# Kernel optimization log

Hardware: AMD Instinct MI355X
Metric: run time of the kernel (lower is better)

## Reference

```python
import math
import jax, jax.numpy as jnp
from jax import lax
import numpy as np

C, H, W, N, K = 256, 64, 64, 16, 7

def setup_inputs() -> dict:
    key = jax.random.key(0)
    k0, k1, k2, k3, k4 = jax.random.split(key, 5)
    x = jax.random.normal(k0, (N, C, H, W), dtype=jnp.float32)
    p_2_w = 0.02 * jax.random.normal(k1, (1, C, H, 1), dtype=jnp.float32)
    # nn.Conv2d(c, c, (1,5), groups=1, bias=False) -> weight [c, c, 1, 5]
    fan_in = C * 1 * 5
    bound = 1.0 / math.sqrt(fan_in)
    p_3_w = jax.random.uniform(k2, (C, C, 1, 5), dtype=jnp.float32, minval=-bound, maxval=bound)
    p_4_w = 0.02 * jax.random.normal(k3, (1, C, K, 1, 1), dtype=jnp.float32)
    p_6_w = jax.random.uniform(k4, (K, 1), dtype=jnp.float32, minval=-7.0, maxval=7.0)
    return {"x": x, "p_2_w": p_2_w, "p_3_w": p_3_w, "p_4_w": p_4_w, "p_6_w": p_6_w}

def reference(x, p_2_w, p_3_w, p_4_w, p_6_w):
    n, c, h, w = x.shape
    k = p_4_w.shape[2]  # 7 taps
    pad = (k - 1) // 2
    # F.unfold with kernel (1,7), pad (0,3): stack 7 width-shifted copies -> [n,c,7,h,w]
    xp = jnp.pad(x, ((0, 0), (0, 0), (0, 0), (pad, pad)))
    t_1 = jnp.stack([xp[..., i:i + w] for i in range(k)], axis=2)
    # per-(channel,row) scaling then dense 1x5 conv
    t_2 = p_2_w * x
    t_3 = lax.conv_general_dilated(
        t_2, p_3_w, window_strides=(1, 1), padding=[(0, 0), (2, 2)],
        dimension_numbers=("NCHW", "OIHW", "NCHW"))
    # weighted tap-sum: (p_4_w * t_1) contracted over taps with p_6_w[:,0]
    t_4 = p_4_w * t_1
    t_6 = jnp.einsum("nckhw,kf->ncfhw", t_4, p_6_w)[:, :, 0]  # [n,c,h,w]
    t_5 = jax.nn.relu(x)
    s = h * w
    # channel-attention matrix [n,c,c]
    t_7 = jnp.einsum("ncs,nds->ncd", t_3.reshape(n, c, s), t_6.reshape(n, c, s))
    t_7 = t_7 * (1.0 / math.sqrt(s))
    # bmm(t_5^T, t_7) -> [n,s,d]; permuting to [n,d,h,w] == einsum 'ncs,ncd->nds'
    out = jnp.einsum("ncs,ncd->nds", t_5.reshape(n, c, s), t_7)
    out = out * (1.0 / math.sqrt(c))
    return out.reshape(n, c, h, w)
```

## Files before the change

### kernel.cpp

```cpp
#include <hip/hip_runtime.h>
#include <hip/hip_bf16.h>

typedef __attribute__((ext_vector_type(8))) short bf16x8;
typedef __attribute__((ext_vector_type(4))) float f32x4;

#define NB 16
#define CD 256
#define HD 64
#define WD 64
#define WP 68
#define SD 4096
#define KU 1280

__device__ __forceinline__ void gload16(const void* g, void* lds) {
  __builtin_amdgcn_global_load_lds(
      (const __attribute__((address_space(1))) unsigned int*)g,
      (__attribute__((address_space(3))) unsigned int*)lds, 16, 0, 0);
}

__global__ __launch_bounds__(256) void prep_w3(const float* __restrict__ p3,
                                               __hip_bfloat16* __restrict__ A) {
  int id = blockIdx.x * 256 + threadIdx.x;
  if (id >= CD * KU) return;
  int o = id / KU;
  int r = id - o * KU;
  int j = r >> 8;
  int c = r & 255;
  A[id] = __float2bfloat16(p3[(o * CD + c) * 5 + j]);
}

__global__ __launch_bounds__(256) void prep_x(const float* __restrict__ x,
                                              const float* __restrict__ p2,
                                              const float* __restrict__ p4,
                                              const float* __restrict__ p6,
                                              __hip_bfloat16* __restrict__ t2p,
                                              __hip_bfloat16* __restrict__ t5T,
                                              __hip_bfloat16* __restrict__ t6) {
  int h = blockIdx.x;
  int c0 = blockIdx.y * 64;
  int n = blockIdx.z;
  __shared__ float xl[64][67];
  __shared__ float p2l[64];
  __shared__ float wtl[64][8];
  int t = threadIdx.x;

  if (t < 64) p2l[t] = p2[(c0 + t) * HD + h];
  for (int idx = t; idx < 448; idx += 256) {
    int c = idx / 7, k = idx - c * 7;
    wtl[c][k] = p4[(c0 + c) * 7 + k] * p6[k];
  }

  {
    int cq = t >> 4;
    int w4 = (t & 15) * 4;
#pragma unroll
    for (int cc = 0; cc < 4; ++cc) {
      int cl = cc * 16 + cq;
      const float4 xv = *reinterpret_cast<const float4*>(
          &x[(((size_t)n * CD + c0 + cl) * HD + h) * WD + w4]);
      xl[cl][w4 + 0] = xv.x;
      xl[cl][w4 + 1] = xv.y;
      xl[cl][w4 + 2] = xv.z;
      xl[cl][w4 + 3] = xv.w;
    }
  }
  __syncthreads();

  __hip_bfloat16* t2pn = t2p + (size_t)n * HD * WP * CD;
#pragma unroll
  for (int ii = 0; ii < 2; ++ii) {
    int w = (t >> 3) + ii * 32;
    int cb = (t & 7) * 8;
    __hip_bfloat16 o2[8], o5[8];
#pragma unroll
    for (int j = 0; j < 8; ++j) {
      float xv = xl[cb + j][w];
      o5[j] = __float2bfloat16(fmaxf(xv, 0.f));
      o2[j] = __float2bfloat16(p2l[cb + j] * xv);
    }
    size_t s = (size_t)h * 64 + w;
    *reinterpret_cast<bf16x8*>(&t5T[((size_t)n * SD + s) * CD + c0 + cb]) =
        *reinterpret_cast<const bf16x8*>(o5);
    *reinterpret_cast<bf16x8*>(&t2pn[((size_t)h * WP + w + 2) * CD + c0 + cb]) =
        *reinterpret_cast<const bf16x8*>(o2);
  }
  if (t < 32) {
    int pi = t >> 3;
    int wp = (pi < 2) ? pi : pi + 64;
    int cb = (t & 7) * 8;
    bf16x8 z = (bf16x8){0, 0, 0, 0, 0, 0, 0, 0};
    *reinterpret_cast<bf16x8*>(&t2pn[((size_t)h * WP + wp) * CD + c0 + cb]) = z;
  }

#pragma unroll
  for (int ii = 0; ii < 2; ++ii) {
    int cl = (t >> 3) + ii * 32;
    int w8 = (t & 7) * 8;
    float hx[14];
#pragma unroll
    for (int m = 0; m < 14; ++m) {
      int wi = w8 - 3 + m;
      hx[m] = (wi >= 0 && wi < 64) ? xl[cl][wi] : 0.f;
    }
    float wt[7];
#pragma unroll
    for (int k = 0; k < 7; ++k) wt[k] = wtl[cl][k];
    __hip_bfloat16 o6[8];
#pragma unroll
    for (int u = 0; u < 8; ++u) {
      float acc = 0.f;
#pragma unroll
      for (int k = 0; k < 7; ++k) acc += wt[k] * hx[u + k];
      o6[u] = __float2bfloat16(acc);
    }
    *reinterpret_cast<bf16x8*>(&t6[((size_t)n * CD + c0 + cl) * SD + h * 64 + w8]) =
        *reinterpret_cast<const bf16x8*>(o6);
  }
}

__global__ __launch_bounds__(256) void gemm_b(const __hip_bfloat16* __restrict__ A,
                                              const __hip_bfloat16* __restrict__ t2p,
                                              __hip_bfloat16* __restrict__ t3) {
  __shared__ __align__(16) __hip_bfloat16 lA[128 * 32];
  __shared__ __align__(16) __hip_bfloat16 lB[128 * 32];
  int n = blockIdx.z;
  int ob = blockIdx.y;
  int sb = blockIdx.x;
  int t = threadIdx.x;
  int wave = t >> 6, lane = t & 63;
  int wm = wave >> 1, wn = wave & 1;
  int l16 = lane & 15, lg = lane >> 4;
  int o0 = ob * 128;
  int s0 = sb * 128;
  const __hip_bfloat16* t2pn = t2p + (size_t)n * HD * WP * CD;

  int srow = t >> 2;
  int scol = (t & 3) * 8;
  const __hip_bfloat16* gA0 = A + (size_t)(o0 + srow) * KU + scol;
  const __hip_bfloat16* gA1 = A + (size_t)(o0 + srow + 64) * KU + scol;
  int sr0 = s0 + srow, sr1 = s0 + srow + 64;
  const __hip_bfloat16* gB0 = t2pn + (size_t)(sr0 + 4 * (sr0 >> 6)) * CD + scol;
  const __hip_bfloat16* gB1 = t2pn + (size_t)(sr1 + 4 * (sr1 >> 6)) * CD + scol;
  __hip_bfloat16* lAd0 = &lA[t * 8];
  __hip_bfloat16* lAd1 = &lA[t * 8 + 64 * 32];
  __hip_bfloat16* lBd0 = &lB[t * 8];
  __hip_bfloat16* lBd1 = &lB[t * 8 + 64 * 32];

  f32x4 acc[4][4];
#pragma unroll
  for (int mi = 0; mi < 4; ++mi)
#pragma unroll
    for (int ni = 0; ni < 4; ++ni) acc[mi][ni] = (f32x4){0.f, 0.f, 0.f, 0.f};

  gload16(gA0, lAd0);
  gload16(gA1, lAd1);
  gload16(gB0, lBd0);
  gload16(gB1, lBd1);

  for (int k = 0; k < 40; ++k) {
    __syncthreads();
    bf16x8 a[4], b[4];
#pragma unroll
    for (int mi = 0; mi < 4; ++mi)
      a[mi] = *reinterpret_cast<const bf16x8*>(&lA[(wm * 64 + mi * 16 + l16) * 32 + lg * 8]);
#pragma unroll
    for (int ni = 0; ni < 4; ++ni)
      b[ni] = *reinterpret_cast<const bf16x8*>(&lB[(wn * 64 + ni * 16 + l16) * 32 + lg * 8]);
#pragma unroll
    for (int mi = 0; mi < 4; ++mi)
#pragma unroll
      for (int ni = 0; ni < 4; ++ni)
        acc[mi][ni] = __builtin_amdgcn_mfma_f32_16x16x32_bf16(a[mi], b[ni], acc[mi][ni], 0, 0, 0);
    __syncthreads();
    if (k < 39) {
      int kk = (k + 1) * 32;
      gload16(gA0 + kk, lAd0);
      gload16(gA1 + kk, lAd1);
      gload16(gB0 + kk, lBd0);
      gload16(gB1 + kk, lBd1);
    }
  }

  __hip_bfloat16* t3n = t3 + (size_t)n * CD * SD;
#pragma unroll
  for (int mi = 0; mi < 4; ++mi)
#pragma unroll
    for (int ni = 0; ni < 4; ++ni) {
      int col = s0 + wn * 64 + ni * 16 + l16;
      int row0 = o0 + wm * 64 + mi * 16 + lg * 4;
#pragma unroll
      for (int r = 0; r < 4; ++r)
        t3n[(size_t)(row0 + r) * SD + col] = __float2bfloat16(acc[mi][ni][r]);
    }
}

__global__ __launch_bounds__(256) void gemm_c_part(const __hip_bfloat16* __restrict__ t6,
                                                   const __hip_bfloat16* __restrict__ t3,
                                                   float* __restrict__ P4) {
  __shared__ __align__(16) __hip_bfloat16 lA[64 * 64];
  __shared__ __align__(16) __hip_bfloat16 lB[64 * 64];
  int bx = blockIdx.x;
  int cbk = bx & 3, kc = bx >> 2;
  int db = blockIdx.y;
  int n = blockIdx.z;
  int t = threadIdx.x;
  int wave = t >> 6, lane = t & 63;
  int wm = wave >> 1, wn = wave & 1;
  int l16 = lane & 15, lg = lane >> 4;
  int d0 = db * 64;
  int c0 = cbk * 64;
  int kbase = kc * 1024;
  const __hip_bfloat16* An = t6 + (size_t)n * CD * SD + kbase;
  const __hip_bfloat16* Bn = t3 + (size_t)n * CD * SD + kbase;

  int srow = t >> 3;
  int scol = (t & 7) * 8;
  const __hip_bfloat16* gA0 = An + (size_t)(d0 + srow) * SD + scol;
  const __hip_bfloat16* gA1 = An + (size_t)(d0 + srow + 32) * SD + scol;
  const __hip_bfloat16* gB0 = Bn + (size_t)(c0 + srow) * SD + scol;
  const __hip_bfloat16* gB1 = Bn + (size_t)(c0 + srow + 32) * SD + scol;
  __hip_bfloat16* lAd0 = &lA[t * 8];
  __hip_bfloat16* lAd1 = &lA[t * 8 + 32 * 64];
  __hip_bfloat16* lBd0 = &lB[t * 8];
  __hip_bfloat16* lBd1 = &lB[t * 8 + 32 * 64];

  f32x4 acc[2][2];
#pragma unroll
  for (int mi = 0; mi < 2; ++mi)
#pragma unroll
    for (int ni = 0; ni < 2; ++ni) acc[mi][ni] = (f32x4){0.f, 0.f, 0.f, 0.f};

  gload16(gA0, lAd0);
  gload16(gA1, lAd1);
  gload16(gB0, lBd0);
  gload16(gB1, lBd1);

  for (int k = 0; k < 16; ++k) {
    __syncthreads();
#pragma unroll
    for (int ks = 0; ks < 2; ++ks) {
      bf16x8 a[2], b[2];
#pragma unroll
      for (int mi = 0; mi < 2; ++mi)
        a[mi] = *reinterpret_cast<const bf16x8*>(&lA[(wm * 32 + mi * 16 + l16) * 64 + ks * 32 + lg * 8]);
#pragma unroll
      for (int ni = 0; ni < 2; ++ni)
        b[ni] = *reinterpret_cast<const bf16x8*>(&lB[(wn * 32 + ni * 16 + l16) * 64 + ks * 32 + lg * 8]);
#pragma unroll
      for (int mi = 0; mi < 2; ++mi)
#pragma unroll
        for (int ni = 0; ni < 2; ++ni)
          acc[mi][ni] = __builtin_amdgcn_mfma_f32_16x16x32_bf16(a[mi], b[ni], acc[mi][ni], 0, 0, 0);
    }
    __syncthreads();
    if (k < 15) {
      int kk = (k + 1) * 64;
      gload16(gA0 + kk, lAd0);
      gload16(gA1 + kk, lAd1);
      gload16(gB0 + kk, lBd0);
      gload16(gB1 + kk, lBd1);
    }
  }

  float* Pn = P4 + ((size_t)kc * NB + n) * CD * CD;
#pragma unroll
  for (int mi = 0; mi < 2; ++mi)
#pragma unroll
    for (int ni = 0; ni < 2; ++ni) {
      int col = c0 + wn * 32 + ni * 16 + l16;
      int row0 = d0 + wm * 32 + mi * 16 + lg * 4;
#pragma unroll
      for (int r = 0; r < 4; ++r)
        Pn[(size_t)(row0 + r) * CD + col] = acc[mi][ni][r];
    }
}

__global__ __launch_bounds__(256) void reduce_P(const float* __restrict__ P4,
                                                __hip_bfloat16* __restrict__ P) {
  size_t i = ((size_t)blockIdx.x * 256 + threadIdx.x) * 4;
  const size_t stride = (size_t)NB * CD * CD;
  float4 a = *reinterpret_cast<const float4*>(P4 + i);
  float4 b = *reinterpret_cast<const float4*>(P4 + stride + i);
  float4 c = *reinterpret_cast<const float4*>(P4 + 2 * stride + i);
  float4 d = *reinterpret_cast<const float4*>(P4 + 3 * stride + i);
  __hip_bfloat16 o[4];
  o[0] = __float2bfloat16((a.x + b.x + c.x + d.x) * 0.015625f);
  o[1] = __float2bfloat16((a.y + b.y + c.y + d.y) * 0.015625f);
  o[2] = __float2bfloat16((a.z + b.z + c.z + d.z) * 0.015625f);
  o[3] = __float2bfloat16((a.w + b.w + c.w + d.w) * 0.015625f);
  *reinterpret_cast<short4*>(&P[i]) = *reinterpret_cast<const short4*>(o);
}

__global__ __launch_bounds__(256) void gemm_d(const __hip_bfloat16* __restrict__ P,
                                              const __hip_bfloat16* __restrict__ t5T,
                                              float* __restrict__ out) {
  __shared__ __align__(16) __hip_bfloat16 lA[128 * 32];
  __shared__ __align__(16) __hip_bfloat16 lB[128 * 32];
  int n = blockIdx.z;
  int db = blockIdx.y;
  int sb = blockIdx.x;
  int t = threadIdx.x;
  int wave = t >> 6, lane = t & 63;
  int wm = wave >> 1, wn = wave & 1;
  int l16 = lane & 15, lg = lane >> 4;
  int d0 = db * 128;
  int s0 = sb * 128;
  const __hip_bfloat16* An = P + (size_t)n * CD * CD;
  const __hip_bfloat16* Bn = t5T + (size_t)n * SD * CD;

  int srow = t >> 2;
  int scol = (t & 3) * 8;
  const __hip_bfloat16* gA0 = An + (size_t)(d0 + srow) * CD + scol;
  const __hip_bfloat16* gA1 = An + (size_t)(d0 + srow + 64) * CD + scol;
  const __hip_bfloat16* gB0 = Bn + (size_t)(s0 + srow) * CD + scol;
  const __hip_bfloat16* gB1 = Bn + (size_t)(s0 + srow + 64) * CD + scol;
  __hip_bfloat16* lAd0 = &lA[t * 8];
  __hip_bfloat16* lAd1 = &lA[t * 8 + 64 * 32];
  __hip_bfloat16* lBd0 = &lB[t * 8];
  __hip_bfloat16* lBd1 = &lB[t * 8 + 64 * 32];

  f32x4 acc[4][4];
#pragma unroll
  for (int mi = 0; mi < 4; ++mi)
#pragma unroll
    for (int ni = 0; ni < 4; ++ni) acc[mi][ni] = (f32x4){0.f, 0.f, 0.f, 0.f};

  gload16(gA0, lAd0);
  gload16(gA1, lAd1);
  gload16(gB0, lBd0);
  gload16(gB1, lBd1);

  for (int k = 0; k < 8; ++k) {
    __syncthreads();
    bf16x8 a[4], b[4];
#pragma unroll
    for (int mi = 0; mi < 4; ++mi)
      a[mi] = *reinterpret_cast<const bf16x8*>(&lA[(wm * 64 + mi * 16 + l16) * 32 + lg * 8]);
#pragma unroll
    for (int ni = 0; ni < 4; ++ni)
      b[ni] = *reinterpret_cast<const bf16x8*>(&lB[(wn * 64 + ni * 16 + l16) * 32 + lg * 8]);
#pragma unroll
    for (int mi = 0; mi < 4; ++mi)
#pragma unroll
      for (int ni = 0; ni < 4; ++ni)
        acc[mi][ni] = __builtin_amdgcn_mfma_f32_16x16x32_bf16(a[mi], b[ni], acc[mi][ni], 0, 0, 0);
    __syncthreads();
    if (k < 7) {
      int kk = (k + 1) * 32;
      gload16(gA0 + kk, lAd0);
      gload16(gA1 + kk, lAd1);
      gload16(gB0 + kk, lBd0);
      gload16(gB1 + kk, lBd1);
    }
  }

  float* outn = out + (size_t)n * CD * SD;
#pragma unroll
  for (int mi = 0; mi < 4; ++mi)
#pragma unroll
    for (int ni = 0; ni < 4; ++ni) {
      int col = s0 + wn * 64 + ni * 16 + l16;
      int row0 = d0 + wm * 64 + mi * 16 + lg * 4;
#pragma unroll
      for (int r = 0; r < 4; ++r)
        outn[(size_t)(row0 + r) * SD + col] = acc[mi][ni][r] * 0.0625f;
    }
}

extern "C" void kernel_launch(void* const* d_in, const int* in_sizes, int n_in,
                              void* d_out, int out_size, void* d_ws, size_t ws_size,
                              hipStream_t stream) {
  const float* x = (const float*)d_in[0];
  const float* p2 = (const float*)d_in[1];
  const float* p3 = (const float*)d_in[2];
  const float* p4 = (const float*)d_in[3];
  const float* p6 = (const float*)d_in[4];

  char* ws = (char*)d_ws;
  size_t off = 0;
  __hip_bfloat16* A = (__hip_bfloat16*)(ws + off);
  off += (size_t)CD * KU * 2;
  size_t t2p_off = off;
  __hip_bfloat16* t2p = (__hip_bfloat16*)(ws + off);
  off += (size_t)NB * HD * WP * CD * 2;
  __hip_bfloat16* t5T = (__hip_bfloat16*)(ws + off);
  off += (size_t)NB * SD * CD * 2;
  __hip_bfloat16* t6 = (__hip_bfloat16*)(ws + off);
  off += (size_t)NB * CD * SD * 2;
  __hip_bfloat16* t3 = (__hip_bfloat16*)(ws + off);
  off += (size_t)NB * CD * SD * 2;
  float* P4 = (float*)(ws + t2p_off);
  __hip_bfloat16* P = (__hip_bfloat16*)(ws + t2p_off + (size_t)4 * NB * CD * CD * 4);

  float* out = (float*)d_out;

  prep_w3<<<dim3((CD * KU + 255) / 256), 256, 0, stream>>>(p3, A);
  prep_x<<<dim3(HD, 4, NB), 256, 0, stream>>>(x, p2, p4, p6, t2p, t5T, t6);
  gemm_b<<<dim3(32, 2, NB), 256, 0, stream>>>(A, t2p, t3);
  gemm_c_part<<<dim3(16, 4, NB), 256, 0, stream>>>(t6, t3, P4);
  reduce_P<<<dim3((NB * CD * CD / 4) / 256), 256, 0, stream>>>(P4, P);
  gemm_d<<<dim3(32, 2, NB), 256, 0, stream>>>(P, t5T, out);
}
```

Before: 153.8 us.

## Rewrite conv GEMM as 256x256-tile 8-wave kernel with double-buffered swizzled LDS

Replaces the 128x128 gemm_b with gemm_b8, which uses 512 threads per block, a 256x256 output tile covering all 256 output channels, and K steps of 64. LDS is double-buffered and XOR-swizzled. Loads for the next K step are issued in interleaved phases between the four MFMA quadrants, gated by explicit vmcnt waits and barriers, with s_setprio raised around the MFMA bursts. The goal is to hide global-load latency, raise arithmetic intensity and cut LDS bank conflicts. In exchange it needs 128 KB of LDS and heavy register use, and it launches only 256 blocks.

```diff
diff --git a/kernel.cpp b/kernel.cpp
--- a/kernel.cpp
+++ b/kernel.cpp
@@ -118,79 +118,110 @@
   }
 }
 
-__global__ __launch_bounds__(256) void gemm_b(const __hip_bfloat16* __restrict__ A,
-                                              const __hip_bfloat16* __restrict__ t2p,
-                                              __hip_bfloat16* __restrict__ t3) {
-  __shared__ __align__(16) __hip_bfloat16 lA[128 * 32];
-  __shared__ __align__(16) __hip_bfloat16 lB[128 * 32];
-  int n = blockIdx.z;
-  int ob = blockIdx.y;
-  int sb = blockIdx.x;
-  int t = threadIdx.x;
-  int wave = t >> 6, lane = t & 63;
-  int wm = wave >> 1, wn = wave & 1;
-  int l16 = lane & 15, lg = lane >> 4;
-  int o0 = ob * 128;
-  int s0 = sb * 128;
-  const __hip_bfloat16* t2pn = t2p + (size_t)n * HD * WP * CD;
-
-  int srow = t >> 2;
-  int scol = (t & 3) * 8;
-  const __hip_bfloat16* gA0 = A + (size_t)(o0 + srow) * KU + scol;
-  const __hip_bfloat16* gA1 = A + (size_t)(o0 + srow + 64) * KU + scol;
-  int sr0 = s0 + srow, sr1 = s0 + srow + 64;
-  const __hip_bfloat16* gB0 = t2pn + (size_t)(sr0 + 4 * (sr0 >> 6)) * CD + scol;
-  const __hip_bfloat16* gB1 = t2pn + (size_t)(sr1 + 4 * (sr1 >> 6)) * CD + scol;
-  __hip_bfloat16* lAd0 = &lA[t * 8];
-  __hip_bfloat16* lAd1 = &lA[t * 8 + 64 * 32];
-  __hip_bfloat16* lBd0 = &lB[t * 8];
-  __hip_bfloat16* lBd1 = &lB[t * 8 + 64 * 32];
-
-  f32x4 acc[4][4];
-#pragma unroll
-  for (int mi = 0; mi < 4; ++mi)
-#pragma unroll
-    for (int ni = 0; ni < 4; ++ni) acc[mi][ni] = (f32x4){0.f, 0.f, 0.f, 0.f};
-
-  gload16(gA0, lAd0);
-  gload16(gA1, lAd1);
-  gload16(gB0, lBd0);
-  gload16(gB1, lBd1);
-
-  for (int k = 0; k < 40; ++k) {
-    __syncthreads();
-    bf16x8 a[4], b[4];
-#pragma unroll
-    for (int mi = 0; mi < 4; ++mi)
-      a[mi] = *reinterpret_cast<const bf16x8*>(&lA[(wm * 64 + mi * 16 + l16) * 32 + lg * 8]);
-#pragma unroll
-    for (int ni = 0; ni < 4; ++ni)
-      b[ni] = *reinterpret_cast<const bf16x8*>(&lB[(wn * 64 + ni * 16 + l16) * 32 + lg * 8]);
-#pragma unroll
-    for (int mi = 0; mi < 4; ++mi)
-#pragma unroll
-      for (int ni = 0; ni < 4; ++ni)
-        acc[mi][ni] = __builtin_amdgcn_mfma_f32_16x16x32_bf16(a[mi], b[ni], acc[mi][ni], 0, 0, 0);
-    __syncthreads();
-    if (k < 39) {
-      int kk = (k + 1) * 32;
-      gload16(gA0 + kk, lAd0);
-      gload16(gA1 + kk, lAd1);
-      gload16(gB0 + kk, lBd0);
-      gload16(gB1 + kk, lBd1);
-    }
-  }
+#define STAGE_A(c, kt, d)                                                              \
+  gload16(Ab + (size_t)((c) * 64 + wv * 8 + (lane >> 3)) * 2560 + (kt) * 128 + cbsrc,  \
+          (char*)lds + (d) * 65536 + (c) * 8192 + wv * 1024)
+#define STAGE_B(j, kt, d)                                                              \
+  gload16(t2pb + (size_t)(s0 + (j) * 64 + wv * 8 + (lane >> 3) + 4 * (sb * 4 + (j))) * 512 + \
+                     (kt) * 128 + cbsrc,                                               \
+          (char*)lds + (d) * 65536 + 32768 + (j) * 8192 + wv * 1024)
+
+#define QUAD(d, MH, NH)                                                                \
+  do {                                                                                 \
+    const __hip_bfloat16* pA =                                                         \
+        lds + (d) * 32768 + (wm * 128 + (MH) * 64 + l16) * 64;                         \
+    const __hip_bfloat16* pB =                                                         \
+        lds + (d) * 32768 + 16384 + (wn * 64 + (NH) * 32 + l16) * 64;                  \
+    _Pragma("unroll") for (int ks = 0; ks < 2; ++ks) {                                 \
+      int cb = ks * 32 + cbsw;                                                         \
+      bf16x8 av[4], bv[2];                                                             \
+      _Pragma("unroll") for (int mf = 0; mf < 4; ++mf)                                 \
+          av[mf] = *reinterpret_cast<const bf16x8*>(pA + mf * 1024 + cb);              \
+      _Pragma("unroll") for (int nf = 0; nf < 2; ++nf)                                 \
+          bv[nf] = *reinterpret_cast<const bf16x8*>(pB + nf * 1024 + cb);              \
+      __builtin_amdgcn_s_setprio(1);                                                   \
+      _Pragma("unroll") for (int mf = 0; mf < 4; ++mf)                                 \
+          _Pragma("unroll") for (int nf = 0; nf < 2; ++nf)                             \
+              acc[(MH) * 4 + mf][(NH) * 2 + nf] = __builtin_amdgcn_mfma_f32_16x16x32_bf16( \
+                  av[mf], bv[nf], acc[(MH) * 4 + mf][(NH) * 2 + nf], 0, 0, 0);         \
+      __builtin_amdgcn_s_setprio(0);                                                   \
+    }                                                                                  \
+  } while (0)
+
+#define VMWAIT(N) asm volatile("s_waitcnt vmcnt(" #N ")" ::: "memory")
+#define BARRIER() __builtin_amdgcn_s_barrier()
+
+__global__ __launch_bounds__(512, 2) void gemm_b8(const __hip_bfloat16* __restrict__ A,
+                                                  const __hip_bfloat16* __restrict__ t2p,
+                                                  __hip_bfloat16* __restrict__ t3) {
+  __shared__ __align__(16) __hip_bfloat16 lds[65536];
+  const int n = blockIdx.z;
+  const int sb = blockIdx.x;
+  const int t = threadIdx.x;
+  const int wv = t >> 6, lane = t & 63;
+  const int wm = wv >> 2, wn = wv & 3;
+  const int l16 = lane & 15, lg = lane >> 4;
+  const int s0 = sb * 256;
+  const char* Ab = (const char*)A;
+  const char* t2pb = (const char*)(t2p + (size_t)n * HD * WP * CD);
+  const int cbsrc = ((lane & 7) * 16) ^ (lane & 32);
+  const int cbsw = (lg * 8) ^ ((l16 & 4) << 2);
+
+  f32x4 acc[8][4];
+#pragma unroll
+  for (int i = 0; i < 8; ++i)
+#pragma unroll
+    for (int j = 0; j < 4; ++j) acc[i][j] = (f32x4){0.f, 0.f, 0.f, 0.f};
+
+  STAGE_B(0, 0, 0); STAGE_B(1, 0, 0); STAGE_B(2, 0, 0); STAGE_B(3, 0, 0);
+  STAGE_A(0, 0, 0); STAGE_A(2, 0, 0); STAGE_A(1, 0, 0); STAGE_A(3, 0, 0);
+
+  for (int kt = 0; kt < 19; ++kt) {
+    const int cur = kt & 1, nxt = cur ^ 1, kn = kt + 1;
+    STAGE_B(0, kn, nxt); STAGE_B(1, kn, nxt);
+    VMWAIT(4);
+    BARRIER();
+    QUAD(cur, 0, 0);
+    BARRIER();
+    STAGE_B(2, kn, nxt); STAGE_B(3, kn, nxt);
+    BARRIER();
+    QUAD(cur, 0, 1);
+    BARRIER();
+    STAGE_A(0, kn, nxt); STAGE_A(2, kn, nxt);
+    VMWAIT(6);
+    BARRIER();
+    QUAD(cur, 1, 0);
+    BARRIER();
+    STAGE_A(1, kn, nxt); STAGE_A(3, kn, nxt);
+    BARRIER();
+    QUAD(cur, 1, 1);
+    BARRIER();
+  }
+  VMWAIT(2);
+  BARRIER();
+  QUAD(1, 0, 0);
+  BARRIER();
+  BARRIER();
+  QUAD(1, 0, 1);
+  BARRIER();
+  VMWAIT(0);
+  BARRIER();
+  QUAD(1, 1, 0);
+  BARRIER();
+  BARRIER();
+  QUAD(1, 1, 1);
+  BARRIER();
 
   __hip_bfloat16* t3n = t3 + (size_t)n * CD * SD;
 #pragma unroll
-  for (int mi = 0; mi < 4; ++mi)
-#pragma unroll
-    for (int ni = 0; ni < 4; ++ni) {
-      int col = s0 + wn * 64 + ni * 16 + l16;
-      int row0 = o0 + wm * 64 + mi * 16 + lg * 4;
+  for (int im = 0; im < 8; ++im)
+#pragma unroll
+    for (int in = 0; in < 4; ++in) {
+      int row0 = wm * 128 + im * 16 + lg * 4;
+      int col = s0 + wn * 64 + in * 16 + l16;
 #pragma unroll
       for (int r = 0; r < 4; ++r)
-        t3n[(size_t)(row0 + r) * SD + col] = __float2bfloat16(acc[mi][ni][r]);
+        t3n[(size_t)(row0 + r) * SD + col] = __float2bfloat16(acc[im][in][r]);
     }
 }
 
@@ -396,7 +427,7 @@
 
   prep_w3<<<dim3((CD * KU + 255) / 256), 256, 0, stream>>>(p3, A);
   prep_x<<<dim3(HD, 4, NB), 256, 0, stream>>>(x, p2, p4, p6, t2p, t5T, t6);
-  gemm_b<<<dim3(32, 2, NB), 256, 0, stream>>>(A, t2p, t3);
+  gemm_b8<<<dim3(16, 1, NB), 512, 0, stream>>>(A, t2p, t3);
   gemm_c_part<<<dim3(16, 4, NB), 256, 0, stream>>>(t6, t3, P4);
   reduce_P<<<dim3((NB * CD * CD / 4) / 256), 256, 0, stream>>>(P4, P);
   gemm_d<<<dim3(32, 2, NB), 256, 0, stream>>>(P, t5T, out);
```

Result: faster. 145.8 us (-5.2%).
